# Kernel tuning notes

Hardware: AMD Instinct MI355X
Metric: run time of the kernel (lower is better)

Reference implementation:

```python
import jax, jax.numpy as jnp
import numpy as np

GROUPS = 32  # from analyze_enhance_linear_ops(4096, 4096, 0.05): smallest divisor g with 1/g <= 0.05


def setup_inputs() -> dict:
    key = jax.random.key(0)
    k1, k2, k3, k4, k5 = jax.random.split(key, 5)
    B, S, D_in, D_out = 4, 2048, 4096, 4096
    ig = D_out // GROUPS  # 128
    x = jax.random.normal(k1, (B, S, D_in), dtype=jnp.float32)
    W = jax.random.normal(k2, (D_out, D_in), dtype=jnp.float32) * 0.02
    b = jax.random.normal(k3, (D_out,), dtype=jnp.float32) * 0.02
    Wg = jax.random.normal(k4, (GROUPS, ig, ig), dtype=jnp.float32) * 0.02
    bg = jax.random.normal(k5, (GROUPS, ig), dtype=jnp.float32) * 0.02
    return {"x": x, "W": W, "b": b, "Wg": Wg, "bg": bg}


def reference(x, W, b, Wg, bg):
    # original_linear: dense GEMM, torch Linear layout W[out, in]
    y = jnp.einsum('bsi,oi->bso', x, W) + b            # [B, S, D_out]
    # GroupedLinear: block-diagonal transform over groups of size out_group
    B, S, D = y.shape
    G, og, ig = Wg.shape
    yg = y.reshape(B, S, G, ig)                        # split into groups
    out = jnp.einsum('bsgi,goi->bsgo', yg, Wg) + bg    # per-group small GEMM + bias
    return out.reshape(B, S, D)                        # cat along feature dim
```

## Files before the change

kernel.cpp:

```cpp
#include <hip/hip_runtime.h>
#include <hip/hip_bf16.h>
#include <stdint.h>

typedef float f32x4 __attribute__((ext_vector_type(4)));
typedef float f32x16 __attribute__((ext_vector_type(16)));
typedef short s16x8 __attribute__((ext_vector_type(8)));
typedef unsigned int u32x2 __attribute__((ext_vector_type(2)));
typedef unsigned int u32x4 __attribute__((ext_vector_type(4)));

#define MDIM 8192
#define NDIM 4096
#define KDIM 4096
#define NKT  64

__device__ __forceinline__ unsigned pkbf(float lo, float hi) {
  unsigned short l = __builtin_bit_cast(unsigned short, __float2bfloat16(lo));
  unsigned short h = __builtin_bit_cast(unsigned short, __float2bfloat16(hi));
  return ((unsigned)h << 16) | (unsigned)l;
}

__device__ __forceinline__ void gload16(const void* g, void* l) {
  __builtin_amdgcn_global_load_lds((const __attribute__((address_space(1))) int*)g,
                                   (__attribute__((address_space(3))) int*)l, 16, 0, 0);
}

__global__ __launch_bounds__(256) void conv_tile(
    const float* __restrict__ X, const float* __restrict__ W,
    s16x8* __restrict__ wsA, s16x8* __restrict__ wsB) {
  __shared__ char lds[32768];
  const int b = blockIdx.x;
  const int tid = threadIdx.x;
  const float* src;
  s16x8* dst;
  int bi;
  if (b < 32 * NKT) { src = X; dst = wsA; bi = b; }
  else              { src = W; dst = wsB; bi = b - 32 * NKT; }
  const int rt = bi >> 6;
  const int kt = bi & 63;
  const int fr = tid >> 4;
  const int c4 = (tid & 15) * 4;
  const int h = c4 >> 5;
  const int ks2 = (c4 >> 4) & 1;
  const int lh = (c4 & 15) >> 3;
  const int e2 = (c4 & 7) * 2;
  #pragma unroll
  for (int f = 0; f < 16; ++f) {
    const int row = f * 16 + fr;
    f32x4 v = *(const f32x4*)(src + ((size_t)rt * 256 + row) * KDIM + kt * 64 + c4);
    u32x2 p = { pkbf(v[0], v[1]), pkbf(v[2], v[3]) };
    const int frag = (h * 2 + ks2) * 8 + (f >> 1);
    const int lane = lh * 32 + (f & 1) * 16 + fr;
    *(u32x2*)(lds + frag * 1024 + lane * 16 + e2) = p;
  }
  __syncthreads();
  const size_t ob = (size_t)bi * 2048;
  #pragma unroll
  for (int i = 0; i < 8; ++i)
    dst[ob + i * 256 + tid] = *(const s16x8*)(lds + (i * 256 + tid) * 16);
}

__global__ __launch_bounds__(512, 2) void gemm256(
    const s16x8* __restrict__ wsA, const s16x8* __restrict__ wsB,
    const float* __restrict__ bias, const float* __restrict__ Wg,
    const float* __restrict__ bg, float* __restrict__ out) {
  extern __shared__ char smem[];
  const int tid = threadIdx.x;
  const int lane = tid & 63;
  const int wid = tid >> 6;
  const int wr = wid >> 2;
  const int wc = wid & 3;
  const int c32 = lane & 31;
  const int q5 = lane >> 5;

  const int bid = blockIdx.x;
  const int swz = (bid & 7) * 64 + (bid >> 3);
  const int bm = swz >> 4;
  const int bn = swz & 15;

  const char* wsAb = (const char*)wsA + ((size_t)bm << 21);
  const char* wsBb = (const char*)wsB + ((size_t)bn << 21);

  auto stageA = [&](int t, int slot) {
    const char* s = wsAb + ((size_t)t << 14) + (wid << 11) + (lane << 4);
    char* d = smem + (slot << 14) + (wid << 11);
    gload16(s, d);
    gload16(s + 1024, d + 1024);
  };

  const char* aRd = smem + (wr << 12) + (lane << 4);

  f32x16 acc[4][2];
  #pragma unroll
  for (int m = 0; m < 4; ++m)
    #pragma unroll
    for (int n = 0; n < 2; ++n) acc[m][n] = (f32x16)0.0f;

  s16x8 af[4], bE[2], bO[2];

  const char* bAddr = wsBb + ((wc * 2) << 10) + (lane << 4);

  stageA(0, 0);
  stageA(1, 1);
  #pragma unroll
  for (int n = 0; n < 2; ++n)
    bE[n] = *(const s16x8*)(bAddr + ((size_t)0 << 13) + (n << 10));
  asm volatile("s_waitcnt vmcnt(2)" ::: "memory");
  __builtin_amdgcn_s_barrier();

  #pragma clang loop unroll(disable)
  for (int t = 0; t < 128; ++t) {
    const int tn = (t + 2 < 128) ? t + 2 : 127;
    const size_t k1 = 2 * t + 1;
    const size_t k2 = (2 * t + 2 < 256) ? 2 * t + 2 : 255;
    const int slot = t & 3;
    stageA(tn, (t + 2) & 3);
    #pragma unroll
    for (int n = 0; n < 2; ++n)
      bO[n] = *(const s16x8*)(bAddr + (k1 << 13) + (n << 10));
    #pragma unroll
    for (int m = 0; m < 4; ++m)
      af[m] = *(const s16x8*)(aRd + (slot << 14) + (m << 10));
    asm volatile("s_waitcnt vmcnt(4)" ::: "memory");
    __builtin_amdgcn_s_barrier();
    __builtin_amdgcn_s_setprio(1);
    #pragma unroll
    for (int m = 0; m < 4; ++m) {
      #pragma unroll
      for (int n = 0; n < 2; ++n)
        acc[m][n] = __builtin_amdgcn_mfma_f32_32x32x16_bf16(af[m], bE[n], acc[m][n], 0, 0, 0);
    }
    __builtin_amdgcn_s_setprio(0);
    #pragma unroll
    for (int n = 0; n < 2; ++n)
      bE[n] = *(const s16x8*)(bAddr + (k2 << 13) + (n << 10));
    #pragma unroll
    for (int m = 0; m < 4; ++m)
      af[m] = *(const s16x8*)(aRd + (slot << 14) + 8192 + (m << 10));
    asm volatile("s_waitcnt vmcnt(4)" ::: "memory");
    __builtin_amdgcn_s_barrier();
    __builtin_amdgcn_s_setprio(1);
    #pragma unroll
    for (int m = 0; m < 4; ++m) {
      #pragma unroll
      for (int n = 0; n < 2; ++n)
        acc[m][n] = __builtin_amdgcn_mfma_f32_32x32x16_bf16(af[m], bO[n], acc[m][n], 0, 0, 0);
    }
    __builtin_amdgcn_s_setprio(0);
  }

  asm volatile("s_waitcnt vmcnt(0)" ::: "memory");
  asm volatile("s_waitcnt lgkmcnt(0)" ::: "memory");
  __builtin_amdgcn_s_barrier();

  float bv[2];
  #pragma unroll
  for (int n = 0; n < 2; ++n) bv[n] = bias[bn * 256 + wc * 64 + n * 32 + c32];

  {
    const int e2 = (c32 & 7) * 2;
    const int lh = (c32 >> 3) & 1;
    #pragma unroll
    for (int m = 0; m < 4; ++m) {
      const int Mf = wr * 4 + m;
      #pragma unroll
      for (int n = 0; n < 2; ++n) {
        const int Kc = wc * 4 + n * 2 + (c32 >> 4);
        char* base = smem + (Mf * 16 + Kc) * 1024 + lh * 512 + e2;
        #pragma unroll
        for (int r = 0; r < 16; ++r) {
          const int rl = (r & 3) + 8 * (r >> 2) + 4 * q5;
          const float y = acc[m][n][r] + bv[n];
          *(unsigned short*)(base + rl * 16) =
              __builtin_bit_cast(unsigned short, __float2bfloat16(y));
        }
      }
    }
  }
  asm volatile("s_waitcnt lgkmcnt(0)" ::: "memory");
  __builtin_amdgcn_s_barrier();

  const int g = bn * 2 + (wc >> 1);
  const float* wgb = Wg + (size_t)g * 16384;
  f32x16 acc2[4][2];
  #pragma unroll
  for (int m = 0; m < 4; ++m)
    #pragma unroll
    for (int n = 0; n < 2; ++n) acc2[m][n] = (f32x16)0.0f;

  #pragma unroll
  for (int ks = 0; ks < 8; ++ks) {
    const int Kc = (wc >> 1) * 8 + ks;
    s16x8 af2[4];
    #pragma unroll
    for (int m = 0; m < 4; ++m)
      af2[m] = *(const s16x8*)(smem + ((wr * 4 + m) * 16 + Kc) * 1024 + lane * 16);
    #pragma unroll
    for (int n = 0; n < 2; ++n) {
      const int ocl = (wc & 1) * 64 + n * 32 + c32;
      const float* wp = wgb + ocl * 128 + ks * 16 + q5 * 8;
      f32x4 w0 = *(const f32x4*)wp;
      f32x4 w1 = *(const f32x4*)(wp + 4);
      u32x4 pw = { pkbf(w0[0], w0[1]), pkbf(w0[2], w0[3]),
                   pkbf(w1[0], w1[1]), pkbf(w1[2], w1[3]) };
      const s16x8 bfw = __builtin_bit_cast(s16x8, pw);
      #pragma unroll
      for (int m = 0; m < 4; ++m)
        acc2[m][n] = __builtin_amdgcn_mfma_f32_32x32x16_bf16(af2[m], bfw, acc2[m][n], 0, 0, 0);
    }
  }

  float bgv[2];
  #pragma unroll
  for (int n = 0; n < 2; ++n) bgv[n] = bg[bn * 256 + wc * 64 + n * 32 + c32];

  #pragma unroll
  for (int m = 0; m < 4; ++m) {
    #pragma unroll
    for (int n = 0; n < 2; ++n) {
      const int col = bn * 256 + wc * 64 + n * 32 + c32;
      #pragma unroll
      for (int r = 0; r < 16; ++r) {
        const size_t row = (size_t)bm * 256 + wr * 128 + m * 32
                         + (r & 3) + 8 * (r >> 2) + 4 * q5;
        out[row * NDIM + col] = acc2[m][n][r] + bgv[n];
      }
    }
  }
}

extern "C" void kernel_launch(void* const* d_in, const int* in_sizes, int n_in,
                              void* d_out, int out_size, void* d_ws, size_t ws_size,
                              hipStream_t stream) {
  const float* X    = (const float*)d_in[0];
  const float* W    = (const float*)d_in[1];
  const float* bias = (const float*)d_in[2];
  const float* Wg   = (const float*)d_in[3];
  const float* bg   = (const float*)d_in[4];
  float* out = (float*)d_out;

  s16x8* wsA = (s16x8*)d_ws;
  s16x8* wsB = wsA + ((size_t)MDIM * KDIM / 8);

  hipFuncSetAttribute(reinterpret_cast<const void*>(gemm256),
                      hipFuncAttributeMaxDynamicSharedMemorySize, 131072);

  conv_tile<<<dim3(3072), dim3(256), 0, stream>>>(X, W, wsA, wsB);
  gemm256<<<dim3(512), dim3(512), 131072, stream>>>(wsA, wsB, bias, Wg, bg, out);
}
```

Baseline: 340.5 us.

## Stage B tiles through LDS with async loads instead of direct global reads

```diff
diff --git a/kernel.cpp b/kernel.cpp
--- a/kernel.cpp
+++ b/kernel.cpp
@@ -80,14 +80,18 @@
   const char* wsAb = (const char*)wsA + ((size_t)bm << 21);
   const char* wsBb = (const char*)wsB + ((size_t)bn << 21);
 
-  auto stageA = [&](int t, int slot) {
-    const char* s = wsAb + ((size_t)t << 14) + (wid << 11) + (lane << 4);
-    char* d = smem + (slot << 14) + (wid << 11);
-    gload16(s, d);
-    gload16(s + 1024, d + 1024);
+  auto stage = [&](int t, int slot) {
+    const char* sa = wsAb + ((size_t)t << 14) + (wid << 11) + (lane << 4);
+    const char* sb = wsBb + ((size_t)t << 14) + (wid << 11) + (lane << 4);
+    char* d = smem + (slot << 15) + (wid << 11);
+    gload16(sa, d);
+    gload16(sa + 1024, d + 1024);
+    gload16(sb, d + 16384);
+    gload16(sb + 1024, d + 16384 + 1024);
   };
 
-  const char* aRd = smem + (wr << 12) + (lane << 4);
+  const char* aRd = smem + ((wr * 4) << 10) + (lane << 4);
+  const char* bRd = smem + 16384 + ((wc * 2) << 10) + (lane << 4);
 
   f32x16 acc[4][2];
   #pragma unroll
@@ -95,57 +99,37 @@
     #pragma unroll
     for (int n = 0; n < 2; ++n) acc[m][n] = (f32x16)0.0f;
 
-  s16x8 af[4], bE[2], bO[2];
-
-  const char* bAddr = wsBb + ((wc * 2) << 10) + (lane << 4);
-
-  stageA(0, 0);
-  stageA(1, 1);
-  #pragma unroll
-  for (int n = 0; n < 2; ++n)
-    bE[n] = *(const s16x8*)(bAddr + ((size_t)0 << 13) + (n << 10));
-  asm volatile("s_waitcnt vmcnt(2)" ::: "memory");
-  __builtin_amdgcn_s_barrier();
+  s16x8 af[4], bfr[2];
+
+  stage(0, 0);
+  stage(1, 1);
 
   #pragma clang loop unroll(disable)
   for (int t = 0; t < 128; ++t) {
     const int tn = (t + 2 < 128) ? t + 2 : 127;
-    const size_t k1 = 2 * t + 1;
-    const size_t k2 = (2 * t + 2 < 256) ? 2 * t + 2 : 255;
-    const int slot = t & 3;
-    stageA(tn, (t + 2) & 3);
-    #pragma unroll
-    for (int n = 0; n < 2; ++n)
-      bO[n] = *(const s16x8*)(bAddr + (k1 << 13) + (n << 10));
-    #pragma unroll
-    for (int m = 0; m < 4; ++m)
-      af[m] = *(const s16x8*)(aRd + (slot << 14) + (m << 10));
-    asm volatile("s_waitcnt vmcnt(4)" ::: "memory");
+    stage(tn, (t + 2) & 3);
+    asm volatile("s_waitcnt vmcnt(8)" ::: "memory");
     __builtin_amdgcn_s_barrier();
-    __builtin_amdgcn_s_setprio(1);
-    #pragma unroll
-    for (int m = 0; m < 4; ++m) {
+    const int so = (t & 3) << 15;
+    #pragma unroll
+    for (int ks = 0; ks < 2; ++ks) {
       #pragma unroll
       for (int n = 0; n < 2; ++n)
-        acc[m][n] = __builtin_amdgcn_mfma_f32_32x32x16_bf16(af[m], bE[n], acc[m][n], 0, 0, 0);
-    }
-    __builtin_amdgcn_s_setprio(0);
-    #pragma unroll
-    for (int n = 0; n < 2; ++n)
-      bE[n] = *(const s16x8*)(bAddr + (k2 << 13) + (n << 10));
-    #pragma unroll
-    for (int m = 0; m < 4; ++m)
-      af[m] = *(const s16x8*)(aRd + (slot << 14) + 8192 + (m << 10));
-    asm volatile("s_waitcnt vmcnt(4)" ::: "memory");
-    __builtin_amdgcn_s_barrier();
-    __builtin_amdgcn_s_setprio(1);
-    #pragma unroll
-    for (int m = 0; m < 4; ++m) {
-      #pragma unroll
-      for (int n = 0; n < 2; ++n)
-        acc[m][n] = __builtin_amdgcn_mfma_f32_32x32x16_bf16(af[m], bO[n], acc[m][n], 0, 0, 0);
-    }
-    __builtin_amdgcn_s_setprio(0);
+        bfr[n] = *(const s16x8*)(bRd + so + ks * 8192 + (n << 10));
+      #pragma unroll
+      for (int m = 0; m < 4; ++m)
+        af[m] = *(const s16x8*)(aRd + so + ks * 8192 + (m << 10));
+      asm volatile("s_waitcnt lgkmcnt(0)" ::: "memory");
+      __builtin_amdgcn_sched_barrier(0);
+      __builtin_amdgcn_s_setprio(1);
+      #pragma unroll
+      for (int m = 0; m < 4; ++m) {
+        #pragma unroll
+        for (int n = 0; n < 2; ++n)
+          acc[m][n] = __builtin_amdgcn_mfma_f32_32x32x16_bf16(af[m], bfr[n], acc[m][n], 0, 0, 0);
+      }
+      __builtin_amdgcn_s_setprio(0);
+    }
   }
 
   asm volatile("s_waitcnt vmcnt(0)" ::: "memory");
```

New measurement: 313.9 us. 1.08x faster.
